# Optimization experiments

Hardware: AMD Instinct MI355X
Metric: run time of the kernel (lower is better)

The kernel has to match this reference:

```python
import jax, jax.numpy as jnp
import numpy as np
import itertools

N_GRAPHS = 64
NODES_PER_GRAPH = 16
N_NODES = N_GRAPHS * NODES_PER_GRAPH  # 1024


def conv2d(x, w, b, stride=1):
    # x: [N, Cin, H, W], w: [Cout, Cin, 3, 3], padding=1 (same as torch Conv2d(...,3,stride,1))
    y = jax.lax.conv_general_dilated(
        x, w, (stride, stride), ((1, 1), (1, 1)),
        dimension_numbers=("NCHW", "OIHW", "NCHW"))
    return y + b[None, :, None, None]


def lrelu(x):
    return jax.nn.leaky_relu(x, 0.1)


def conv_mpn(x, edges, c1w, c1b, c2w, c2b, c3w, c3b):
    # ConvMPN: gather neighbour / non-neighbour node features, scatter_add to dst,
    # concat on channel dim, then 3 convs (no activation in between, as in source).
    n = x.shape[0]
    a, s, b = edges[:, 0], edges[:, 1], edges[:, 2]
    src = jnp.concatenate([a, b])  # bidirectional, matches torch cat([e0,e2]) / cat([e2,e0])
    dst = jnp.concatenate([b, a])
    pos = jnp.concatenate([s > 0, s > 0]).astype(x.dtype)
    neg = jnp.concatenate([s < 0, s < 0]).astype(x.dtype)
    gathered = x[src]  # [2E, C, H, W]
    neigh = jax.ops.segment_sum(gathered * pos[:, None, None, None], dst, num_segments=n)
    non = jax.ops.segment_sum(gathered * neg[:, None, None, None], dst, num_segments=n)
    h = jnp.concatenate([x, neigh, non], axis=1)  # [N, 3C, H, W]
    h = conv2d(h, c1w, c1b)
    h = conv2d(h, c2w, c2b)
    h = conv2d(h, c3w, c3b)
    return h


def setup_inputs() -> dict:
    key = jax.random.key(0)
    ks = iter(jax.random.split(key, 40))

    def p(shape):
        fan_in = int(np.prod(shape[1:])) if len(shape) > 1 else shape[0]
        return jax.random.normal(next(ks), shape, dtype=jnp.float32) / np.sqrt(fan_in)

    x = jax.random.normal(next(ks), (N_NODES, 32, 32), dtype=jnp.float32)
    t = jax.random.normal(next(ks), (N_NODES, 10), dtype=jnp.float32)

    # complete graph per sample; sign +/-1 marks neighbour vs non-neighbour
    pairs = np.array(list(itertools.combinations(range(NODES_PER_GRAPH), 2)))  # (120, 2)
    offs = np.arange(N_GRAPHS)[:, None] * NODES_PER_GRAPH
    aa = (pairs[None, :, 0] + offs).ravel()
    bb = (pairs[None, :, 1] + offs).ravel()
    rng = np.random.RandomState(0)
    sign = rng.choice(np.array([-1, 1]), size=aa.shape[0])
    edges = jnp.asarray(np.stack([aa, sign, bb], axis=1).astype(np.int64))
    nd_to_sample = jnp.asarray(np.repeat(np.arange(N_GRAPHS), NODES_PER_GRAPH).astype(np.int64))

    inp = {
        "x": x, "t": t, "edges": edges, "nd_to_sample": nd_to_sample,
        "w_t": p((8192, 10)), "b_t": jnp.zeros((8192,), jnp.float32),
        "c1w": p((16, 9, 3, 3)), "c1b": jnp.zeros((16,), jnp.float32),
        "c2w": p((16, 16, 3, 3)), "c2b": jnp.zeros((16,), jnp.float32),
        "c3w": p((16, 16, 3, 3)), "c3b": jnp.zeros((16,), jnp.float32),
        "m1c1w": p((32, 48, 3, 3)), "m1c1b": jnp.zeros((32,), jnp.float32),
        "m1c2w": p((32, 32, 3, 3)), "m1c2b": jnp.zeros((32,), jnp.float32),
        "m1c3w": p((16, 32, 3, 3)), "m1c3b": jnp.zeros((16,), jnp.float32),
        "ds1w": p((16, 16, 3, 3)), "ds1b": jnp.zeros((16,), jnp.float32),
        "m2c1w": p((32, 48, 3, 3)), "m2c1b": jnp.zeros((32,), jnp.float32),
        "m2c2w": p((32, 32, 3, 3)), "m2c2b": jnp.zeros((32,), jnp.float32),
        "m2c3w": p((16, 32, 3, 3)), "m2c3b": jnp.zeros((16,), jnp.float32),
        "ds2w": p((16, 16, 3, 3)), "ds2b": jnp.zeros((16,), jnp.float32),
        "d1w": p((256, 16, 3, 3)), "d1b": jnp.zeros((256,), jnp.float32),
        "d2w": p((128, 256, 3, 3)), "d2b": jnp.zeros((128,), jnp.float32),
        "d3w": p((128, 128, 3, 3)), "d3b": jnp.zeros((128,), jnp.float32),
        "pw": p((1, 128)), "pb": jnp.zeros((1,), jnp.float32),
    }
    return inp


def reference(x, t, edges, nd_to_sample,
              w_t, b_t, c1w, c1b, c2w, c2b, c3w, c3b,
              m1c1w, m1c1b, m1c2w, m1c2b, m1c3w, m1c3b, ds1w, ds1b,
              m2c1w, m2c1b, m2c2w, m2c2b, m2c3w, m2c3b, ds2w, ds2b,
              d1w, d1b, d2w, d2b, d3w, d3b, pw, pb):
    h = x.reshape(-1, 1, 32, 32)
    tt = (t @ w_t.T + b_t).reshape(-1, 8, 32, 32)
    h = jnp.concatenate([h, tt], axis=1)  # [N, 9, 32, 32]
    h = lrelu(conv2d(h, c1w, c1b))
    h = lrelu(conv2d(h, c2w, c2b))
    h = lrelu(conv2d(h, c3w, c3b))
    h = conv_mpn(h, edges, m1c1w, m1c1b, m1c2w, m1c2b, m1c3w, m1c3b)
    h = lrelu(conv2d(h, ds1w, ds1b, stride=2))  # 32 -> 16
    h = conv_mpn(h, edges, m2c1w, m2c1b, m2c2w, m2c2b, m2c3w, m2c3b)
    h = lrelu(conv2d(h, ds2w, ds2b, stride=2))  # 16 -> 8
    h = lrelu(conv2d(h, d1w, d1b, stride=2))    # 8 -> 4
    h = lrelu(conv2d(h, d2w, d2b, stride=2))    # 4 -> 2
    h = lrelu(conv2d(h, d3w, d3b, stride=2))    # 2 -> 1
    h = h.reshape(-1, h.shape[1])               # [N, 128]
    pooled = jax.ops.segment_sum(h, nd_to_sample, num_segments=N_GRAPHS)  # add_pool
    return pooled @ pw.T + pb                    # [B, 1]
```

## Files before the change

### kernel.cpp

```cpp
#include <hip/hip_runtime.h>
#include <hip/hip_bf16.h>


#define N_NODES   1024
#define N_GRAPHS  64

typedef __hip_bfloat16 bf16;
typedef __attribute__((ext_vector_type(8)))  short  short8;
typedef __attribute__((ext_vector_type(16))) float  f32x16;

__device__ __forceinline__ float bf2f(unsigned short s) {
    union { unsigned u; float f; } x; x.u = ((unsigned)s) << 16; return x.f;
}
__device__ __forceinline__ unsigned short f2bf(float f) {
    __hip_bfloat16 h = __float2bfloat16(f);
    return *reinterpret_cast<unsigned short*>(&h);
}
__device__ __forceinline__ uint4 pack8(const float* f) {
    uint4 r;
    r.x = f2bf(f[0]) | ((unsigned)f2bf(f[1]) << 16);
    r.y = f2bf(f[2]) | ((unsigned)f2bf(f[3]) << 16);
    r.z = f2bf(f[4]) | ((unsigned)f2bf(f[5]) << 16);
    r.w = f2bf(f[6]) | ((unsigned)f2bf(f[7]) << 16);
    return r;
}

template<int N>
__device__ __forceinline__ void zacc(f32x16* a) {
    #pragma unroll
    for (int i = 0; i < N; ++i)
        #pragma unroll
        for (int e = 0; e < 16; ++e) a[i][e] = 0.f;
}

template<int TPW, int NW>
__device__ __forceinline__ void mfma_rr32(
    const short* lds, int inbase, int zch,
    const unsigned short* wfb, int kkstride_sh,
    f32x16* acc, int wid, int lane)
{
    const int pxl = lane & 31, kg = lane >> 5;
    short8 wfr[9];
    #pragma unroll
    for (int kk = 0; kk < 9; ++kk)
        wfr[kk] = *(const short8*)(wfb + (size_t)kk * kkstride_sh + lane * 8);
    const int r0 = wid * TPW;
    #pragma unroll
    for (int ir = 0; ir < TPW + 2; ++ir) {
        int iy = r0 - 1 + ir;
        if (iy < 0 || iy > 31) continue;
        #pragma unroll
        for (int dx = 0; dx < 3; ++dx) {
            int ix = pxl + dx - 1;
            bool ok = (unsigned)ix < 32u;
            int chunk = ok ? (inbase + kg * 1024 + iy * 32 + ix) : zch;
            short8 B = *(const short8*)(lds + (size_t)chunk * 8);
            #pragma unroll
            for (int dy = -1; dy <= 1; ++dy) {
                constexpr int dummy = 0; (void)dummy;
                int a = ir - 1 - dy;
                if (a < 0 || a >= TPW) continue;
                acc[a] = __builtin_amdgcn_mfma_f32_32x32x16_bf16(
                    wfr[(dy + 1) * 3 + dx], B, acc[a], 0, 0, 0);
            }
        }
    }
}

template<int WIN, int WOUT, int STRIDE, int TPW, int TILES, int NW>
__device__ __forceinline__ void mfma_phase(
    const short* lds, int inbase, int zch,
    const unsigned short* wfb, int kkstride_sh,
    f32x16* acc, int wid, int lane)
{
    constexpr int NPI = WIN * WIN;
    const int pxl = lane & 31, kg = lane >> 5;
    short8 wfr[9];
    #pragma unroll
    for (int kk = 0; kk < 9; ++kk)
        wfr[kk] = *(const short8*)(wfb + (size_t)kk * kkstride_sh + lane * 8);
    #pragma unroll
    for (int t = 0; t < TPW; ++t) {
        int tile = wid * TPW + t;
        if (NW * TPW > TILES && tile >= TILES) continue;
        int oy, ox;
        if (WOUT == 32)      { oy = tile;                  ox = pxl;      }
        else if (WOUT == 16) { oy = tile * 2 + (pxl >> 4); ox = pxl & 15; }
        else                 { oy = tile * 4 + (pxl >> 3); ox = pxl & 7;  }
        #pragma unroll
        for (int kk = 0; kk < 9; ++kk) {
            int iy = STRIDE * oy + kk / 3 - 1, ix = STRIDE * ox + kk % 3 - 1;
            bool ok = ((unsigned)iy < (unsigned)WIN) && ((unsigned)ix < (unsigned)WIN);
            int chunk = ok ? (inbase + kg * NPI + iy * WIN + ix) : zch;
            acc[t] = __builtin_amdgcn_mfma_f32_32x32x16_bf16(
                wfr[kk], *(const short8*)(lds + (size_t)chunk * 8), acc[t], 0, 0, 0);
        }
    }
}

template<int WOUT, int COUT, int RELU, int TPW, int TILES, int NW, bool TOGLOBAL>
__device__ __forceinline__ void conv_epi(
    short* lds, int outbase, unsigned short* gout,
    const float* __restrict__ bias, const f32x16* acc, int wid, int lane)
{
    constexpr int NPO = WOUT * WOUT;
    const int pxl = lane & 31, kg = lane >> 5;
    #pragma unroll
    for (int t = 0; t < TPW; ++t) {
        int tile = wid * TPW + t;
        if (NW * TPW > TILES && tile >= TILES) continue;
        int oy, ox;
        if (WOUT == 32)      { oy = tile;                  ox = pxl;      }
        else if (WOUT == 16) { oy = tile * 2 + (pxl >> 4); ox = pxl & 15; }
        else                 { oy = tile * 4 + (pxl >> 3); ox = pxl & 7;  }
        int opx = oy * WOUT + ox;
        #pragma unroll
        for (int q = 0; q < COUT / 8; ++q) {
            unsigned short u[4];
            #pragma unroll
            for (int j = 0; j < 4; ++j) {
                int co = q * 8 + kg * 4 + j;
                float v = acc[t][4 * q + j] + bias[co];
                if (RELU) v = (v >= 0.f) ? v : 0.1f * v;
                u[j] = f2bf(v);
            }
            uint2 pk;
            pk.x = u[0] | ((unsigned)u[1] << 16);
            pk.y = u[2] | ((unsigned)u[3] << 16);
            if constexpr (TOGLOBAL)
                *(uint2*)(gout + ((size_t)q * NPO + opx) * 8 + kg * 4) = pk;
            else
                *(uint2*)(lds + ((size_t)(outbase + q * NPO + opx)) * 8 + kg * 4) = pk;
        }
    }
}

__global__ __launch_bounds__(64) void k_build_adj(
    const int* __restrict__ edges, int per_g,
    int* __restrict__ cnt, int* __restrict__ lst)
{
    int n = blockIdx.x * 64 + threadIdx.x;
    if (n >= N_NODES) return;
    int g = n >> 4;
    const int* eg = edges + (size_t)g * per_g * 3;
    int c = 0;
    for (int k = 0; k < per_g; ++k) {
        int a = eg[k * 3 + 0];
        int s = eg[k * 3 + 1];
        int b = eg[k * 3 + 2];
        int other = (a == n) ? b : ((b == n) ? a : -1);
        if (other >= 0 && (other >> 4) == g && c < 16) {
            lst[n * 16 + c] = other | ((s < 0) ? (int)0x80000000 : 0);
            ++c;
        }
    }
    cnt[n] = c;
}

#define N_PREP 14
struct PrepArgs {
    const float* w[N_PREP];
    unsigned short* o[N_PREP];
    int cin[N_PREP], cout[N_PREP], cig[N_PREP], mt[N_PREP], base[N_PREP];
};

__global__ __launch_bounds__(64) void k_prep_all(PrepArgs a)
{
    int b = blockIdx.x;
    int L = 0;
    #pragma unroll
    for (int i = 1; i < N_PREP; ++i) if (b >= a.base[i]) L = i;
    int rel = b - a.base[L];
    int MT = a.mt[L], CIG = a.cig[L];
    int m = rel % MT; rel /= MT;
    int cg = rel % CIG;
    int kk = rel / CIG;
    int Cin = a.cin[L], Cout = a.cout[L];
    int lane = threadIdx.x;
    int co = m * 32 + (lane & 31), kg = lane >> 5;
    float v[8];
    #pragma unroll
    for (int j = 0; j < 8; ++j) {
        int ci = cg * 16 + kg * 8 + j;
        v[j] = (co < Cout && ci < Cin) ? a.w[L][((size_t)co * Cin + ci) * 9 + kk] : 0.f;
    }
    *(uint4*)(a.o[L] + ((size_t)((kk * CIG + cg) * MT + m) * 64 + lane) * 8) = pack8(v);
}

__global__ __launch_bounds__(512) void k_front(
    const float* __restrict__ x, const float* __restrict__ t,
    const float* __restrict__ wt, const float* __restrict__ bt,
    const unsigned short* __restrict__ wf1, const float* __restrict__ b1,
    const unsigned short* __restrict__ wf2, const float* __restrict__ b2,
    const unsigned short* __restrict__ wf3, const float* __restrict__ b3,
    bf16* __restrict__ c3o, int node_base)
{
    __shared__ __align__(16) short lds[4097 * 8];
    __shared__ float s_t[10];
    const int nl = blockIdx.x, n = node_base + nl, tid = threadIdx.x;
    const int wid = tid >> 6, lane = tid & 63;
    if (tid < 10) s_t[tid] = t[n * 10 + tid];
    if (tid < 8)  lds[4096 * 8 + tid] = 0;
    __syncthreads();

    #pragma unroll
    for (int p = 0; p < 2; ++p) {
        int px = tid + p * 512;
        float ch[16];
        ch[0] = x[(size_t)n * 1024 + px];
        #pragma unroll
        for (int c = 1; c <= 8; ++c) {
            int o = (c - 1) * 1024 + px;
            float a = bt[o];
            const float* wr = wt + (size_t)o * 10;
            #pragma unroll
            for (int k = 0; k < 10; ++k) a += wr[k] * s_t[k];
            ch[c] = a;
        }
        #pragma unroll
        for (int c = 9; c < 16; ++c) ch[c] = 0.f;
        *(uint4*)(lds + (size_t)px * 8)          = pack8(ch);
        *(uint4*)(lds + (size_t)(1024 + px) * 8) = pack8(ch + 8);
    }
    __syncthreads();

    f32x16 acc[4];
    zacc<4>(acc);
    mfma_rr32<4, 8>(lds, 0, 4096, wf1, 512, acc, wid, lane);
    conv_epi<32, 16, 1, 4, 32, 8, false>(lds, 2048, nullptr, b1, acc, wid, lane);
    __syncthreads();
    zacc<4>(acc);
    mfma_rr32<4, 8>(lds, 2048, 4096, wf2, 512, acc, wid, lane);
    conv_epi<32, 16, 1, 4, 32, 8, false>(lds, 0, nullptr, b2, acc, wid, lane);
    __syncthreads();
    zacc<4>(acc);
    mfma_rr32<4, 8>(lds, 0, 4096, wf3, 512, acc, wid, lane);
    conv_epi<32, 16, 1, 4, 32, 8, true>(lds, 0,
        (unsigned short*)c3o + (size_t)nl * 16384, b3, acc, wid, lane);
}

__global__ __launch_bounds__(512) void k_mid1(
    const bf16* __restrict__ c3o, const bf16* __restrict__ g1p,
    const unsigned short* __restrict__ wf1, const float* __restrict__ b1,
    const unsigned short* __restrict__ wf2, const float* __restrict__ b2,
    const unsigned short* __restrict__ wf3, const float* __restrict__ b3,
    const unsigned short* __restrict__ wfd, const float* __restrict__ bd,
    bf16* __restrict__ ds1o)
{
    __shared__ __align__(16) short lds[8193 * 8];
    const int nl = blockIdx.x, tid = threadIdx.x;
    const int wid = tid >> 6, lane = tid & 63;
    if (tid < 8) lds[8192 * 8 + tid] = 0;

    uint4* l4 = (uint4*)lds;
    const uint4* s0 = (const uint4*)c3o + (size_t)nl * 2048;
    const uint4* s1 = (const uint4*)g1p + (size_t)nl * 4096;
    const uint4* s2 = s1 + 2048;
    #pragma unroll
    for (int r = 0; r < 4; ++r) l4[tid + r * 512] = s0[tid + r * 512];
    __syncthreads();

    f32x16 acc[4];
    zacc<4>(acc);
    uint4 pf[4];
    #pragma unroll
    for (int r = 0; r < 4; ++r) pf[r] = s1[tid + r * 512];
    mfma_rr32<4, 8>(lds, 0, 8192, wf1, 3 * 512, acc, wid, lane);
    #pragma unroll
    for (int r = 0; r < 4; ++r) l4[2048 + tid + r * 512] = pf[r];
    __syncthreads();
    #pragma unroll
    for (int r = 0; r < 4; ++r) pf[r] = s2[tid + r * 512];
    mfma_rr32<4, 8>(lds, 2048, 8192, wf1 + 512, 3 * 512, acc, wid, lane);
    #pragma unroll
    for (int r = 0; r < 4; ++r) l4[tid + r * 512] = pf[r];
    __syncthreads();
    mfma_rr32<4, 8>(lds, 0, 8192, wf1 + 1024, 3 * 512, acc, wid, lane);
    conv_epi<32, 32, 0, 4, 32, 8, false>(lds, 4096, nullptr, b1, acc, wid, lane);
    __syncthreads();

    zacc<4>(acc);
    mfma_rr32<4, 8>(lds, 4096, 8192, wf2,       2 * 512, acc, wid, lane);
    mfma_rr32<4, 8>(lds, 6144, 8192, wf2 + 512, 2 * 512, acc, wid, lane);
    conv_epi<32, 32, 0, 4, 32, 8, false>(lds, 0, nullptr, b2, acc, wid, lane);
    __syncthreads();

    zacc<4>(acc);
    mfma_rr32<4, 8>(lds, 0,    8192, wf3,       2 * 512, acc, wid, lane);
    mfma_rr32<4, 8>(lds, 2048, 8192, wf3 + 512, 2 * 512, acc, wid, lane);
    conv_epi<32, 16, 0, 4, 32, 8, false>(lds, 4096, nullptr, b3, acc, wid, lane);
    __syncthreads();

    zacc<1>(acc);
    mfma_phase<32, 16, 2, 1, 8, 8>(lds, 4096, 8192, wfd, 512, acc, wid, lane);
    conv_epi<16, 16, 1, 1, 8, 8, true>(lds, 0,
        (unsigned short*)ds1o + (size_t)nl * 4096, bd, acc, wid, lane);
}

__global__ __launch_bounds__(512) void k_mid2(
    const bf16* __restrict__ ds1o, const bf16* __restrict__ g2p,
    const unsigned short* __restrict__ wf1, const float* __restrict__ b1,
    const unsigned short* __restrict__ wf2, const float* __restrict__ b2,
    const unsigned short* __restrict__ wf3, const float* __restrict__ b3,
    const unsigned short* __restrict__ wfd, const float* __restrict__ bd,
    bf16* __restrict__ ds2o)
{
    __shared__ __align__(16) short lds[2049 * 8];
    const int nl = blockIdx.x, tid = threadIdx.x;
    const int wid = tid >> 6, lane = tid & 63;
    if (tid < 8) lds[2048 * 8 + tid] = 0;

    uint4* l4 = (uint4*)lds;
    const uint4* s0 = (const uint4*)ds1o + (size_t)nl * 512;
    const uint4* s1 = (const uint4*)g2p + (size_t)nl * 1024;
    const uint4* s2 = s1 + 512;
    l4[tid] = s0[tid];
    __syncthreads();

    f32x16 acc[1];
    zacc<1>(acc);
    uint4 pf;
    pf = s1[tid];
    mfma_phase<16, 16, 1, 1, 8, 8>(lds, 0, 2048, wf1, 3 * 512, acc, wid, lane);
    l4[512 + tid] = pf;
    __syncthreads();
    pf = s2[tid];
    mfma_phase<16, 16, 1, 1, 8, 8>(lds, 512, 2048, wf1 + 512, 3 * 512, acc, wid, lane);
    l4[tid] = pf;
    __syncthreads();
    mfma_phase<16, 16, 1, 1, 8, 8>(lds, 0, 2048, wf1 + 1024, 3 * 512, acc, wid, lane);
    conv_epi<16, 32, 0, 1, 8, 8, false>(lds, 1024, nullptr, b1, acc, wid, lane);
    __syncthreads();

    zacc<1>(acc);
    mfma_phase<16, 16, 1, 1, 8, 8>(lds, 1024, 2048, wf2,       2 * 512, acc, wid, lane);
    mfma_phase<16, 16, 1, 1, 8, 8>(lds, 1536, 2048, wf2 + 512, 2 * 512, acc, wid, lane);
    conv_epi<16, 32, 0, 1, 8, 8, false>(lds, 0, nullptr, b2, acc, wid, lane);
    __syncthreads();

    zacc<1>(acc);
    mfma_phase<16, 16, 1, 1, 8, 8>(lds, 0,   2048, wf3,       2 * 512, acc, wid, lane);
    mfma_phase<16, 16, 1, 1, 8, 8>(lds, 512, 2048, wf3 + 512, 2 * 512, acc, wid, lane);
    conv_epi<16, 16, 0, 1, 8, 8, false>(lds, 1024, nullptr, b3, acc, wid, lane);
    __syncthreads();

    zacc<1>(acc);
    mfma_phase<16, 8, 2, 1, 2, 8>(lds, 1024, 2048, wfd, 512, acc, wid, lane);
    conv_epi<8, 16, 1, 1, 2, 8, true>(lds, 0,
        (unsigned short*)ds2o + (size_t)nl * 1024, bd, acc, wid, lane);
}

template<int NPIX>
__global__ __launch_bounds__(256) void k_gather2(
    const bf16* __restrict__ in, const int* __restrict__ cnt,
    const int* __restrict__ lst, bf16* __restrict__ out, int node_base)
{
    constexpr int CPN = 2 * NPIX;
    __shared__ __align__(16) uint4 s_in[16 * 128];
    __shared__ int s_pos[16], s_neg[16];

    const int gl = blockIdx.x, sp = blockIdx.y, tid = threadIdx.x;
    const int gn0 = node_base + gl * 16, nl0 = gl * 16;

    if (tid < 16) {
        int c = cnt[gn0 + tid]; if (c > 16) c = 16;
        int pm = 0, nm = 0;
        for (int k = 0; k < c; ++k) {
            int e = lst[(size_t)(gn0 + tid) * 16 + k];
            int sl = (e & 0x7FFFFFFF) - gn0;
            if ((unsigned)sl < 16u) { if (e < 0) nm |= 1 << sl; else pm |= 1 << sl; }
        }
        s_pos[tid] = pm; s_neg[tid] = nm;
    }
    const uint4* in4 = (const uint4*)in;
    for (int i = tid; i < 2048; i += 256) {
        int srcn = i >> 7, chk = i & 127;
        s_in[i] = in4[(size_t)(nl0 + srcn) * CPN + sp * 128 + chk];
    }
    __syncthreads();

    const int dh = tid >> 7, ch = tid & 127;
    int pm[8], nm[8];
    #pragma unroll
    for (int dl = 0; dl < 8; ++dl) {
        pm[dl] = __builtin_amdgcn_readfirstlane(s_pos[dh * 8 + dl]);
        nm[dl] = __builtin_amdgcn_readfirstlane(s_neg[dh * 8 + dl]);
    }

    float aP[8][8], aN[8][8];
    #pragma unroll
    for (int dl = 0; dl < 8; ++dl)
        #pragma unroll
        for (int j = 0; j < 8; ++j) { aP[dl][j] = 0.f; aN[dl][j] = 0.f; }

    for (int s = 0; s < 16; ++s) {
        union { uint4 v; unsigned short u[8]; } q;
        q.v = s_in[s * 128 + ch];
        float f[8];
        #pragma unroll
        for (int j = 0; j < 8; ++j) f[j] = bf2f(q.u[j]);
        #pragma unroll
        for (int dl = 0; dl < 8; ++dl) {
            if ((pm[dl] >> s) & 1) {
                #pragma unroll
                for (int j = 0; j < 8; ++j) aP[dl][j] += f[j];
            }
            if ((nm[dl] >> s) & 1) {
                #pragma unroll
                for (int j = 0; j < 8; ++j) aN[dl][j] += f[j];
            }
        }
    }

    uint4* out4 = (uint4*)out;
    #pragma unroll
    for (int dl = 0; dl < 8; ++dl) {
        int d = nl0 + dh * 8 + dl;
        out4[((size_t)d * 2 + 0) * CPN + sp * 128 + ch] = pack8(aP[dl]);
        out4[((size_t)d * 2 + 1) * CPN + sp * 128 + ch] = pack8(aN[dl]);
    }
}

template<int HIN, int CIG, int COUT, int IPB, int FUSE_POOL>
__global__ __launch_bounds__(256) void k_tail(
    const bf16* __restrict__ in, const unsigned short* __restrict__ wf,
    const float* __restrict__ bias, bf16* __restrict__ out,
    const int* __restrict__ nd, const float* __restrict__ pw,
    float* __restrict__ pool_out, int nc, int node_base)
{
    constexpr int HOUT = HIN / 2, NPO = HOUT * HOUT, NPI = HIN * HIN;
    constexpr int MT  = (COUT + 31) / 32;
    constexpr int NT  = (IPB * NPO) / 32;
    constexpr int TOT = MT * NT;
    constexpr int TPW = TOT / 4;
    static_assert(TOT % 4 == 0, "tile count must divide over 4 waves");
    constexpr int CHUNKS = IPB * 2 * CIG * NPI;
    __shared__ __align__(16) short sbuf[CHUNKS * 8 + 8];

    const int tid = threadIdx.x, wid = tid >> 6, lane = tid & 63;
    const int col = lane & 31, kg = lane >> 5;
    const int img0 = blockIdx.x * IPB;

    {
        const uint4* src = (const uint4*)in + (size_t)img0 * (2 * CIG * NPI);
        uint4* dst = (uint4*)sbuf;
        int nav = nc - img0; if (nav > IPB) nav = IPB;
        int nch = nav * 2 * CIG * NPI;
        uint4 z = {0, 0, 0, 0};
        for (int i = tid; i < CHUNKS; i += 256) dst[i] = (i < nch) ? src[i] : z;
        if (tid < 8) sbuf[CHUNKS * 8 + tid] = 0;
    }
    __syncthreads();

    int imgb[TPW], poff[TPW][9];
    #pragma unroll
    for (int t = 0; t < TPW; ++t) {
        int tl = wid + 4 * t;
        int n  = tl % NT;
        int idx = n * 32 + col;
        int img = idx / NPO, px = idx % NPO;
        imgb[t] = img * (2 * CIG * NPI);
        int oy = px / HOUT, ox = px % HOUT;
        #pragma unroll
        for (int kk = 0; kk < 9; ++kk) {
            int iy = 2 * oy + kk / 3 - 1, ix = 2 * ox + kk % 3 - 1;
            bool ok = ((unsigned)iy < (unsigned)HIN) && ((unsigned)ix < (unsigned)HIN);
            poff[t][kk] = ok ? (iy * HIN + ix) : -1;
        }
    }

    f32x16 acc[TPW];
    #pragma unroll
    for (int t = 0; t < TPW; ++t)
        #pragma unroll
        for (int e = 0; e < 16; ++e) acc[t][e] = 0.f;

    for (int cig = 0; cig < CIG; ++cig) {
        #pragma unroll
        for (int t = 0; t < TPW; ++t) {
            int m = (wid + 4 * t) / NT;
            #pragma unroll
            for (int kk = 0; kk < 9; ++kk) {
                short8 wfr = *(const short8*)(wf +
                    ((size_t)((kk * CIG + cig) * MT + m) * 64 + lane) * 8);
                int chunk = (poff[t][kk] >= 0)
                          ? imgb[t] + (cig * 2 + kg) * NPI + poff[t][kk]
                          : CHUNKS;
                acc[t] = __builtin_amdgcn_mfma_f32_32x32x16_bf16(
                            wfr, *(const short8*)(sbuf + chunk * 8), acc[t], 0, 0, 0);
            }
        }
    }

    #pragma unroll
    for (int t = 0; t < TPW; ++t) {
        int tl = wid + 4 * t;
        int m = tl / NT, n = tl % NT;
        int idx = n * 32 + col;
        int img = idx / NPO, px = idx % NPO;
        bool live = (img0 + img) < nc;
        if (FUSE_POOL) {
            float part = 0.f;
            #pragma unroll
            for (int r = 0; r < 16; ++r) {
                int co = m * 32 + (r & 3) + 8 * (r >> 2) + 4 * kg;
                float v = acc[t][r] + bias[co];
                v = (v >= 0.f) ? v : 0.1f * v;
                part += v * pw[co];
            }
            part += __shfl_xor(part, 32, 64);
            if (kg == 0 && live) {
                int g = nd[node_base + img0 + img];
                if (g < 0) g = 0; if (g >= N_GRAPHS) g = N_GRAPHS - 1;
                atomicAdd(&pool_out[g], part);
            }
        } else if (live) {
            unsigned short* outp = (unsigned short*)out;
            #pragma unroll
            for (int q = 0; q < 4; ++q) {
                if (m * 32 + q * 8 < COUT) {
                    unsigned short u[4];
                    #pragma unroll
                    for (int j = 0; j < 4; ++j) {
                        int co = m * 32 + q * 8 + kg * 4 + j;
                        float v = acc[t][4 * q + j] + bias[co];
                        v = (v >= 0.f) ? v : 0.1f * v;
                        u[j] = f2bf(v);
                    }
                    uint2 pk;
                    pk.x = u[0] | ((unsigned)u[1] << 16);
                    pk.y = u[2] | ((unsigned)u[3] << 16);
                    *(uint2*)(outp + (((size_t)(img0 + img) * (COUT / 8)
                              + (m * 4 + q)) * NPO + px) * 8 + kg * 4) = pk;
                }
            }
        }
    }
}

__global__ void k_init_out(float* out, const float* __restrict__ pb)
{
    int i = threadIdx.x;
    if (i < N_GRAPHS) out[i] = pb[0];
}

extern "C" void kernel_launch(void* const* d_in, const int* in_sizes, int n_in,
                              void* d_out, int out_size, void* d_ws, size_t ws_size,
                              hipStream_t stream)
{
    const float* x     = (const float*)d_in[0];
    const float* t     = (const float*)d_in[1];
    const int*   edges = (const int*)d_in[2];
    const int*   nd    = (const int*)d_in[3];
    const float* w_t   = (const float*)d_in[4];
    const float* b_t   = (const float*)d_in[5];
    const float* c1w   = (const float*)d_in[6];
    const float* c1b   = (const float*)d_in[7];
    const float* c2w   = (const float*)d_in[8];
    const float* c2b   = (const float*)d_in[9];
    const float* c3w   = (const float*)d_in[10];
    const float* c3b   = (const float*)d_in[11];
    const float* m1c1w = (const float*)d_in[12];
    const float* m1c1b = (const float*)d_in[13];
    const float* m1c2w = (const float*)d_in[14];
    const float* m1c2b = (const float*)d_in[15];
    const float* m1c3w = (const float*)d_in[16];
    const float* m1c3b = (const float*)d_in[17];
    const float* ds1w  = (const float*)d_in[18];
    const float* ds1b  = (const float*)d_in[19];
    const float* m2c1w = (const float*)d_in[20];
    const float* m2c1b = (const float*)d_in[21];
    const float* m2c2w = (const float*)d_in[22];
    const float* m2c2b = (const float*)d_in[23];
    const float* m2c3w = (const float*)d_in[24];
    const float* m2c3b = (const float*)d_in[25];
    const float* ds2w  = (const float*)d_in[26];
    const float* ds2b  = (const float*)d_in[27];
    const float* d1w   = (const float*)d_in[28];
    const float* d1b   = (const float*)d_in[29];
    const float* d2w   = (const float*)d_in[30];
    const float* d2b   = (const float*)d_in[31];
    const float* d3w   = (const float*)d_in[32];
    const float* d3b   = (const float*)d_in[33];
    const float* pw    = (const float*)d_in[34];
    const float* pb    = (const float*)d_in[35];
    float* out = (float*)d_out;

    uint8_t* ws = (uint8_t*)d_ws;
    int* adj_cnt = (int*)ws;
    int* adj_lst = (int*)(ws + 4096);
    #define WF(i)  ((unsigned short*)(ws + (128u << 10) + (size_t)(i) * 32768))
    unsigned short* wt_ds1 = (unsigned short*)(ws + (416u  << 10));
    unsigned short* wt_ds2 = (unsigned short*)(ws + (428u  << 10));
    unsigned short* wt_d1  = (unsigned short*)(ws + (440u  << 10));
    unsigned short* wt_d2  = (unsigned short*)(ws + (512u  << 10));
    unsigned short* wt_d3  = (unsigned short*)(ws + (1088u << 10));

    const size_t RESV = 2ull << 20;
    size_t avail = (ws_size > RESV) ? ws_size - RESV : 0;
    int ncap = (int)(avail / (120 * 1024));
    ncap = (ncap / 16) * 16;
    if (ncap < 16) ncap = 16;
    if (ncap > N_NODES) ncap = N_NODES;
    uint8_t* R = ws + RESV;
    #define NB(off_kb) (R + (size_t)(off_kb) * 1024 * ncap)

    bf16*  c3o  = (bf16*)NB(0);
    bf16*  g1p  = (bf16*)NB(32);
    bf16*  ds1o = (bf16*)NB(96);
    bf16*  g2p  = (bf16*)NB(104);
    bf16*  ds2o = (bf16*)NB(0);
    bf16*  d1o  = (bf16*)NB(2);
    bf16*  d2o  = (bf16*)NB(10);

    int nE    = in_sizes[2] / 3;
    int per_g = nE / N_GRAPHS;

    k_build_adj<<<(N_NODES + 63) / 64, 64, 0, stream>>>(edges, per_g, adj_cnt, adj_lst);
    k_init_out<<<1, 64, 0, stream>>>(out, pb);

    {
        PrepArgs pa;
        const float* wsrc[N_PREP] = { c1w, c2w, c3w, m1c1w, m1c2w, m1c3w,
                                      m2c1w, m2c2w, m2c3w, ds1w, ds2w,
                                      d1w, d2w, d3w };
        unsigned short* wdst[N_PREP] = { WF(0), WF(1), WF(2), WF(3), WF(4), WF(5),
                                         WF(6), WF(7), WF(8), wt_ds1, wt_ds2,
                                         wt_d1, wt_d2, wt_d3 };
        int cin_[N_PREP]  = { 9, 16, 16, 48, 32, 32, 48, 32, 32, 16, 16, 16, 256, 128 };
        int cout_[N_PREP] = { 16, 16, 16, 32, 32, 16, 32, 32, 16, 16, 16, 256, 128, 128 };
        int cig_[N_PREP]  = { 1, 1, 1, 3, 2, 2, 3, 2, 2, 1, 1, 1, 16, 8 };
        int mt_[N_PREP]   = { 1, 1, 1, 1, 1, 1, 1, 1, 1, 1, 1, 8, 4, 4 };
        int total = 0;
        for (int i = 0; i < N_PREP; ++i) {
            pa.w[i] = wsrc[i]; pa.o[i] = wdst[i];
            pa.cin[i] = cin_[i]; pa.cout[i] = cout_[i];
            pa.cig[i] = cig_[i]; pa.mt[i] = mt_[i];
            pa.base[i] = total;
            total += 9 * cig_[i] * mt_[i];
        }
        k_prep_all<<<total, 64, 0, stream>>>(pa);
    }

    for (int nb = 0; nb < N_NODES; nb += ncap) {
        int nc = (N_NODES - nb < ncap) ? (N_NODES - nb) : ncap;
        int ng = nc / 16;

        k_front<<<nc, 512, 0, stream>>>(x, t, w_t, b_t,
            WF(0), c1b, WF(1), c2b, WF(2), c3b, c3o, nb);

        k_gather2<1024><<<dim3(ng, 16), 256, 0, stream>>>(c3o, adj_cnt, adj_lst, g1p, nb);

        k_mid1<<<nc, 512, 0, stream>>>(c3o, g1p,
            WF(3), m1c1b, WF(4), m1c2b, WF(5), m1c3b, wt_ds1, ds1b, ds1o);

        k_gather2<256><<<dim3(ng, 4), 256, 0, stream>>>(ds1o, adj_cnt, adj_lst, g2p, nb);

        k_mid2<<<nc, 512, 0, stream>>>(ds1o, g2p,
            WF(6), m2c1b, WF(7), m2c2b, WF(8), m2c3b, wt_ds2, ds2b, ds2o);

        k_tail<8, 1, 256, 4, 0><<<(nc + 3) / 4, 256, 0, stream>>>(
            ds2o, wt_d1, d1b, d1o, nullptr, nullptr, nullptr, nc, nb);
        k_tail<4, 16, 128, 8, 0><<<(nc + 7) / 8, 256, 0, stream>>>(
            d1o, wt_d2, d2b, d2o, nullptr, nullptr, nullptr, nc, nb);
        k_tail<2, 8, 128, 32, 1><<<(nc + 31) / 32, 256, 0, stream>>>(
            d2o, wt_d3, d3b, nullptr, nd, pw, out, nc, nb);
    }
    #undef NB
    #undef WF
}
```

Measured before the change: 285.3 us.

## Fuse tail convs into one kernel, merge setup kernels, use async LDS loads

```diff
diff --git a/kernel.cpp b/kernel.cpp
--- a/kernel.cpp
+++ b/kernel.cpp
@@ -12,17 +12,26 @@
 __device__ __forceinline__ float bf2f(unsigned short s) {
     union { unsigned u; float f; } x; x.u = ((unsigned)s) << 16; return x.f;
 }
-__device__ __forceinline__ unsigned short f2bf(float f) {
-    __hip_bfloat16 h = __float2bfloat16(f);
-    return *reinterpret_cast<unsigned short*>(&h);
+__device__ __forceinline__ unsigned cvtpk(float a, float b) {
+    unsigned r;
+    asm("v_cvt_pk_bf16_f32 %0, %1, %2" : "=v"(r) : "v"(a), "v"(b));
+    return r;
 }
 __device__ __forceinline__ uint4 pack8(const float* f) {
     uint4 r;
-    r.x = f2bf(f[0]) | ((unsigned)f2bf(f[1]) << 16);
-    r.y = f2bf(f[2]) | ((unsigned)f2bf(f[3]) << 16);
-    r.z = f2bf(f[4]) | ((unsigned)f2bf(f[5]) << 16);
-    r.w = f2bf(f[6]) | ((unsigned)f2bf(f[7]) << 16);
+    r.x = cvtpk(f[0], f[1]);
+    r.y = cvtpk(f[2], f[3]);
+    r.z = cvtpk(f[4], f[5]);
+    r.w = cvtpk(f[6], f[7]);
     return r;
+}
+__device__ __forceinline__ void gload16(const void* g, void* l) {
+    __builtin_amdgcn_global_load_lds(
+        reinterpret_cast<const __attribute__((address_space(1))) unsigned*>(
+            reinterpret_cast<uintptr_t>(g)),
+        reinterpret_cast<__attribute__((address_space(3))) unsigned*>(
+            reinterpret_cast<uintptr_t>(l)),
+        16, 0, 0);
 }
 
 template<int N>
@@ -31,40 +40,6 @@
     for (int i = 0; i < N; ++i)
         #pragma unroll
         for (int e = 0; e < 16; ++e) a[i][e] = 0.f;
-}
-
-template<int TPW, int NW>
-__device__ __forceinline__ void mfma_rr32(
-    const short* lds, int inbase, int zch,
-    const unsigned short* wfb, int kkstride_sh,
-    f32x16* acc, int wid, int lane)
-{
-    const int pxl = lane & 31, kg = lane >> 5;
-    short8 wfr[9];
-    #pragma unroll
-    for (int kk = 0; kk < 9; ++kk)
-        wfr[kk] = *(const short8*)(wfb + (size_t)kk * kkstride_sh + lane * 8);
-    const int r0 = wid * TPW;
-    #pragma unroll
-    for (int ir = 0; ir < TPW + 2; ++ir) {
-        int iy = r0 - 1 + ir;
-        if (iy < 0 || iy > 31) continue;
-        #pragma unroll
-        for (int dx = 0; dx < 3; ++dx) {
-            int ix = pxl + dx - 1;
-            bool ok = (unsigned)ix < 32u;
-            int chunk = ok ? (inbase + kg * 1024 + iy * 32 + ix) : zch;
-            short8 B = *(const short8*)(lds + (size_t)chunk * 8);
-            #pragma unroll
-            for (int dy = -1; dy <= 1; ++dy) {
-                constexpr int dummy = 0; (void)dummy;
-                int a = ir - 1 - dy;
-                if (a < 0 || a >= TPW) continue;
-                acc[a] = __builtin_amdgcn_mfma_f32_32x32x16_bf16(
-                    wfr[(dy + 1) * 3 + dx], B, acc[a], 0, 0, 0);
-            }
-        }
-    }
 }
 
 template<int WIN, int WOUT, int STRIDE, int TPW, int TILES, int NW>
@@ -116,45 +91,22 @@
         int opx = oy * WOUT + ox;
         #pragma unroll
         for (int q = 0; q < COUT / 8; ++q) {
-            unsigned short u[4];
+            float v[4];
             #pragma unroll
             for (int j = 0; j < 4; ++j) {
                 int co = q * 8 + kg * 4 + j;
-                float v = acc[t][4 * q + j] + bias[co];
-                if (RELU) v = (v >= 0.f) ? v : 0.1f * v;
-                u[j] = f2bf(v);
+                float x = acc[t][4 * q + j] + bias[co];
+                v[j] = RELU ? ((x >= 0.f) ? x : 0.1f * x) : x;
             }
             uint2 pk;
-            pk.x = u[0] | ((unsigned)u[1] << 16);
-            pk.y = u[2] | ((unsigned)u[3] << 16);
+            pk.x = cvtpk(v[0], v[1]);
+            pk.y = cvtpk(v[2], v[3]);
             if constexpr (TOGLOBAL)
                 *(uint2*)(gout + ((size_t)q * NPO + opx) * 8 + kg * 4) = pk;
             else
                 *(uint2*)(lds + ((size_t)(outbase + q * NPO + opx)) * 8 + kg * 4) = pk;
         }
     }
-}
-
-__global__ __launch_bounds__(64) void k_build_adj(
-    const int* __restrict__ edges, int per_g,
-    int* __restrict__ cnt, int* __restrict__ lst)
-{
-    int n = blockIdx.x * 64 + threadIdx.x;
-    if (n >= N_NODES) return;
-    int g = n >> 4;
-    const int* eg = edges + (size_t)g * per_g * 3;
-    int c = 0;
-    for (int k = 0; k < per_g; ++k) {
-        int a = eg[k * 3 + 0];
-        int s = eg[k * 3 + 1];
-        int b = eg[k * 3 + 2];
-        int other = (a == n) ? b : ((b == n) ? a : -1);
-        if (other >= 0 && (other >> 4) == g && c < 16) {
-            lst[n * 16 + c] = other | ((s < 0) ? (int)0x80000000 : 0);
-            ++c;
-        }
-    }
-    cnt[n] = c;
 }
 
 #define N_PREP 14
@@ -162,29 +114,53 @@
     const float* w[N_PREP];
     unsigned short* o[N_PREP];
     int cin[N_PREP], cout[N_PREP], cig[N_PREP], mt[N_PREP], base[N_PREP];
+    int prep_total;
+    const int* edges; int per_g;
+    int* adj_cnt; int* adj_lst;
+    float* out; const float* pb;
 };
 
-__global__ __launch_bounds__(64) void k_prep_all(PrepArgs a)
+__global__ __launch_bounds__(64) void k_setup(PrepArgs a)
 {
     int b = blockIdx.x;
-    int L = 0;
-    #pragma unroll
-    for (int i = 1; i < N_PREP; ++i) if (b >= a.base[i]) L = i;
-    int rel = b - a.base[L];
-    int MT = a.mt[L], CIG = a.cig[L];
-    int m = rel % MT; rel /= MT;
-    int cg = rel % CIG;
-    int kk = rel / CIG;
-    int Cin = a.cin[L], Cout = a.cout[L];
-    int lane = threadIdx.x;
-    int co = m * 32 + (lane & 31), kg = lane >> 5;
-    float v[8];
-    #pragma unroll
-    for (int j = 0; j < 8; ++j) {
-        int ci = cg * 16 + kg * 8 + j;
-        v[j] = (co < Cout && ci < Cin) ? a.w[L][((size_t)co * Cin + ci) * 9 + kk] : 0.f;
-    }
-    *(uint4*)(a.o[L] + ((size_t)((kk * CIG + cg) * MT + m) * 64 + lane) * 8) = pack8(v);
+    int tid = threadIdx.x;
+    if (b < a.prep_total) {
+        int L = 0;
+        #pragma unroll
+        for (int i = 1; i < N_PREP; ++i) if (b >= a.base[i]) L = i;
+        int rel = b - a.base[L];
+        int MT = a.mt[L], CIG = a.cig[L];
+        int m = rel % MT; rel /= MT;
+        int cg = rel % CIG;
+        int kk = rel / CIG;
+        int Cin = a.cin[L], Cout = a.cout[L];
+        int co = m * 32 + (tid & 31), kg = tid >> 5;
+        float v[8];
+        #pragma unroll
+        for (int j = 0; j < 8; ++j) {
+            int ci = cg * 16 + kg * 8 + j;
+            v[j] = (co < Cout && ci < Cin) ? a.w[L][((size_t)co * Cin + ci) * 9 + kk] : 0.f;
+        }
+        *(uint4*)(a.o[L] + ((size_t)((kk * CIG + cg) * MT + m) * 64 + tid) * 8) = pack8(v);
+    } else if (b < a.prep_total + 16) {
+        int n = (b - a.prep_total) * 64 + tid;
+        int g = n >> 4;
+        const int* eg = a.edges + (size_t)g * a.per_g * 3;
+        int c = 0;
+        for (int k = 0; k < a.per_g; ++k) {
+            int aa = eg[k * 3 + 0];
+            int s  = eg[k * 3 + 1];
+            int bb = eg[k * 3 + 2];
+            int other = (aa == n) ? bb : ((bb == n) ? aa : -1);
+            if (other >= 0 && (other >> 4) == g && c < 16) {
+                a.adj_lst[n * 16 + c] = other | ((s < 0) ? (int)0x80000000 : 0);
+                ++c;
+            }
+        }
+        a.adj_cnt[n] = c;
+    } else {
+        if (tid < N_GRAPHS) a.out[tid] = a.pb[0];
+    }
 }
 
 __global__ __launch_bounds__(512) void k_front(
@@ -226,15 +202,15 @@
 
     f32x16 acc[4];
     zacc<4>(acc);
-    mfma_rr32<4, 8>(lds, 0, 4096, wf1, 512, acc, wid, lane);
+    mfma_phase<32, 32, 1, 4, 32, 8>(lds, 0, 4096, wf1, 512, acc, wid, lane);
     conv_epi<32, 16, 1, 4, 32, 8, false>(lds, 2048, nullptr, b1, acc, wid, lane);
     __syncthreads();
     zacc<4>(acc);
-    mfma_rr32<4, 8>(lds, 2048, 4096, wf2, 512, acc, wid, lane);
+    mfma_phase<32, 32, 1, 4, 32, 8>(lds, 2048, 4096, wf2, 512, acc, wid, lane);
     conv_epi<32, 16, 1, 4, 32, 8, false>(lds, 0, nullptr, b2, acc, wid, lane);
     __syncthreads();
     zacc<4>(acc);
-    mfma_rr32<4, 8>(lds, 0, 4096, wf3, 512, acc, wid, lane);
+    mfma_phase<32, 32, 1, 4, 32, 8>(lds, 0, 4096, wf3, 512, acc, wid, lane);
     conv_epi<32, 16, 1, 4, 32, 8, true>(lds, 0,
         (unsigned short*)c3o + (size_t)nl * 16384, b3, acc, wid, lane);
 }
@@ -265,29 +241,29 @@
     uint4 pf[4];
     #pragma unroll
     for (int r = 0; r < 4; ++r) pf[r] = s1[tid + r * 512];
-    mfma_rr32<4, 8>(lds, 0, 8192, wf1, 3 * 512, acc, wid, lane);
+    mfma_phase<32, 32, 1, 4, 32, 8>(lds, 0, 8192, wf1, 3 * 512, acc, wid, lane);
     #pragma unroll
     for (int r = 0; r < 4; ++r) l4[2048 + tid + r * 512] = pf[r];
     __syncthreads();
     #pragma unroll
     for (int r = 0; r < 4; ++r) pf[r] = s2[tid + r * 512];
-    mfma_rr32<4, 8>(lds, 2048, 8192, wf1 + 512, 3 * 512, acc, wid, lane);
+    mfma_phase<32, 32, 1, 4, 32, 8>(lds, 2048, 8192, wf1 + 512, 3 * 512, acc, wid, lane);
     #pragma unroll
     for (int r = 0; r < 4; ++r) l4[tid + r * 512] = pf[r];
     __syncthreads();
-    mfma_rr32<4, 8>(lds, 0, 8192, wf1 + 1024, 3 * 512, acc, wid, lane);
+    mfma_phase<32, 32, 1, 4, 32, 8>(lds, 0, 8192, wf1 + 1024, 3 * 512, acc, wid, lane);
     conv_epi<32, 32, 0, 4, 32, 8, false>(lds, 4096, nullptr, b1, acc, wid, lane);
     __syncthreads();
 
     zacc<4>(acc);
-    mfma_rr32<4, 8>(lds, 4096, 8192, wf2,       2 * 512, acc, wid, lane);
-    mfma_rr32<4, 8>(lds, 6144, 8192, wf2 + 512, 2 * 512, acc, wid, lane);
+    mfma_phase<32, 32, 1, 4, 32, 8>(lds, 4096, 8192, wf2,       2 * 512, acc, wid, lane);
+    mfma_phase<32, 32, 1, 4, 32, 8>(lds, 6144, 8192, wf2 + 512, 2 * 512, acc, wid, lane);
     conv_epi<32, 32, 0, 4, 32, 8, false>(lds, 0, nullptr, b2, acc, wid, lane);
     __syncthreads();
 
     zacc<4>(acc);
-    mfma_rr32<4, 8>(lds, 0,    8192, wf3,       2 * 512, acc, wid, lane);
-    mfma_rr32<4, 8>(lds, 2048, 8192, wf3 + 512, 2 * 512, acc, wid, lane);
+    mfma_phase<32, 32, 1, 4, 32, 8>(lds, 0,    8192, wf3,       2 * 512, acc, wid, lane);
+    mfma_phase<32, 32, 1, 4, 32, 8>(lds, 2048, 8192, wf3 + 512, 2 * 512, acc, wid, lane);
     conv_epi<32, 16, 0, 4, 32, 8, false>(lds, 4096, nullptr, b3, acc, wid, lane);
     __syncthreads();
 
@@ -373,9 +349,11 @@
         s_pos[tid] = pm; s_neg[tid] = nm;
     }
     const uint4* in4 = (const uint4*)in;
-    for (int i = tid; i < 2048; i += 256) {
+    #pragma unroll
+    for (int k = 0; k < 8; ++k) {
+        int i = tid + k * 256;
         int srcn = i >> 7, chk = i & 127;
-        s_in[i] = in4[(size_t)(nl0 + srcn) * CPN + sp * 128 + chk];
+        gload16(&in4[(size_t)(nl0 + srcn) * CPN + sp * 128 + chk], &s_in[i]);
     }
     __syncthreads();
 
@@ -421,127 +399,157 @@
     }
 }
 
-template<int HIN, int CIG, int COUT, int IPB, int FUSE_POOL>
-__global__ __launch_bounds__(256) void k_tail(
-    const bf16* __restrict__ in, const unsigned short* __restrict__ wf,
-    const float* __restrict__ bias, bf16* __restrict__ out,
+__global__ __launch_bounds__(512) void k_tail3(
+    const bf16* __restrict__ ds2o,
+    const unsigned short* __restrict__ w1, const float* __restrict__ b1,
+    const unsigned short* __restrict__ w2, const float* __restrict__ b2,
+    const unsigned short* __restrict__ w3, const float* __restrict__ b3,
     const int* __restrict__ nd, const float* __restrict__ pw,
-    float* __restrict__ pool_out, int nc, int node_base)
-{
-    constexpr int HOUT = HIN / 2, NPO = HOUT * HOUT, NPI = HIN * HIN;
-    constexpr int MT  = (COUT + 31) / 32;
-    constexpr int NT  = (IPB * NPO) / 32;
-    constexpr int TOT = MT * NT;
-    constexpr int TPW = TOT / 4;
-    static_assert(TOT % 4 == 0, "tile count must divide over 4 waves");
-    constexpr int CHUNKS = IPB * 2 * CIG * NPI;
-    __shared__ __align__(16) short sbuf[CHUNKS * 8 + 8];
-
+    float* __restrict__ out, int node_base)
+{
+    __shared__ __align__(16) short lds[5121 * 8];
+    __shared__ float s_part[4][8];
     const int tid = threadIdx.x, wid = tid >> 6, lane = tid & 63;
     const int col = lane & 31, kg = lane >> 5;
-    const int img0 = blockIdx.x * IPB;
+    const int img0 = blockIdx.x * 8;
+    if (tid < 8) lds[5120 * 8 + tid] = 0;
+
+    const uint4* src = (const uint4*)ds2o + (size_t)img0 * 128;
+    gload16(src + tid,       (uint4*)lds + tid);
+    gload16(src + 512 + tid, (uint4*)lds + 512 + tid);
+    __syncthreads();
 
     {
-        const uint4* src = (const uint4*)in + (size_t)img0 * (2 * CIG * NPI);
-        uint4* dst = (uint4*)sbuf;
-        int nav = nc - img0; if (nav > IPB) nav = IPB;
-        int nch = nav * 2 * CIG * NPI;
-        uint4 z = {0, 0, 0, 0};
-        for (int i = tid; i < CHUNKS; i += 256) dst[i] = (i < nch) ? src[i] : z;
-        if (tid < 8) sbuf[CHUNKS * 8 + tid] = 0;
-    }
-    __syncthreads();
-
-    int imgb[TPW], poff[TPW][9];
-    #pragma unroll
-    for (int t = 0; t < TPW; ++t) {
-        int tl = wid + 4 * t;
-        int n  = tl % NT;
-        int idx = n * 32 + col;
-        int img = idx / NPO, px = idx % NPO;
-        imgb[t] = img * (2 * CIG * NPI);
-        int oy = px / HOUT, ox = px % HOUT;
+        f32x16 acc[4];
+        zacc<4>(acc);
+        #pragma unroll
+        for (int t = 0; t < 4; ++t) {
+            int tl = wid + 8 * t;
+            int m = tl >> 2, n = tl & 3;
+            int idx = n * 32 + col;
+            int img = idx >> 4, px = idx & 15;
+            int oy = px >> 2, ox = px & 3;
+            #pragma unroll
+            for (int kk = 0; kk < 9; ++kk) {
+                int iy = 2 * oy + kk / 3 - 1, ix = 2 * ox + kk % 3 - 1;
+                bool ok = ((unsigned)iy < 8u) && ((unsigned)ix < 8u);
+                int chunk = ok ? (img * 128 + kg * 64 + iy * 8 + ix) : 5120;
+                short8 wfr = *(const short8*)(w1 + ((size_t)(kk * 8 + m) * 64 + lane) * 8);
+                acc[t] = __builtin_amdgcn_mfma_f32_32x32x16_bf16(
+                    wfr, *(const short8*)(lds + (size_t)chunk * 8), acc[t], 0, 0, 0);
+            }
+        }
+        #pragma unroll
+        for (int t = 0; t < 4; ++t) {
+            int tl = wid + 8 * t;
+            int m = tl >> 2, n = tl & 3;
+            int idx = n * 32 + col;
+            int img = idx >> 4, px = idx & 15;
+            #pragma unroll
+            for (int q = 0; q < 4; ++q) {
+                float v[4];
+                #pragma unroll
+                for (int j = 0; j < 4; ++j) {
+                    int co = m * 32 + q * 8 + kg * 4 + j;
+                    float x = acc[t][4 * q + j] + b1[co];
+                    v[j] = (x >= 0.f) ? x : 0.1f * x;
+                }
+                uint2 pk;
+                pk.x = cvtpk(v[0], v[1]);
+                pk.y = cvtpk(v[2], v[3]);
+                *(uint2*)(lds + ((size_t)(1024 + img * 512 + (m * 4 + q) * 16 + px)) * 8
+                          + kg * 4) = pk;
+            }
+        }
+    }
+    __syncthreads();
+
+    {
+        f32x16 acc;
+        #pragma unroll
+        for (int e = 0; e < 16; ++e) acc[e] = 0.f;
+        int img = col >> 2, px = col & 3;
+        int oy = px >> 1, ox = px & 1;
+        int poff[9];
         #pragma unroll
         for (int kk = 0; kk < 9; ++kk) {
             int iy = 2 * oy + kk / 3 - 1, ix = 2 * ox + kk % 3 - 1;
-            bool ok = ((unsigned)iy < (unsigned)HIN) && ((unsigned)ix < (unsigned)HIN);
-            poff[t][kk] = ok ? (iy * HIN + ix) : -1;
-        }
-    }
-
-    f32x16 acc[TPW];
-    #pragma unroll
-    for (int t = 0; t < TPW; ++t)
-        #pragma unroll
-        for (int e = 0; e < 16; ++e) acc[t][e] = 0.f;
-
-    for (int cig = 0; cig < CIG; ++cig) {
-        #pragma unroll
-        for (int t = 0; t < TPW; ++t) {
-            int m = (wid + 4 * t) / NT;
+            bool ok = ((unsigned)iy < 4u) && ((unsigned)ix < 4u);
+            poff[kk] = ok ? (iy * 4 + ix) : -1;
+        }
+        if (wid < 4) {
+            for (int cig = 0; cig < 16; ++cig) {
+                #pragma unroll
+                for (int kk = 0; kk < 9; ++kk) {
+                    short8 wfr = *(const short8*)(w2 +
+                        ((size_t)((kk * 16 + cig) * 4 + wid) * 64 + lane) * 8);
+                    int chunk = (poff[kk] >= 0)
+                              ? 1024 + img * 512 + (cig * 2 + kg) * 16 + poff[kk]
+                              : 5120;
+                    acc = __builtin_amdgcn_mfma_f32_32x32x16_bf16(
+                        wfr, *(const short8*)(lds + (size_t)chunk * 8), acc, 0, 0, 0);
+                }
+            }
+        }
+        __syncthreads();
+        if (wid < 4) {
             #pragma unroll
-            for (int kk = 0; kk < 9; ++kk) {
-                short8 wfr = *(const short8*)(wf +
-                    ((size_t)((kk * CIG + cig) * MT + m) * 64 + lane) * 8);
-                int chunk = (poff[t][kk] >= 0)
-                          ? imgb[t] + (cig * 2 + kg) * NPI + poff[t][kk]
-                          : CHUNKS;
-                acc[t] = __builtin_amdgcn_mfma_f32_32x32x16_bf16(
-                            wfr, *(const short8*)(sbuf + chunk * 8), acc[t], 0, 0, 0);
-            }
-        }
-    }
-
-    #pragma unroll
-    for (int t = 0; t < TPW; ++t) {
-        int tl = wid + 4 * t;
-        int m = tl / NT, n = tl % NT;
-        int idx = n * 32 + col;
-        int img = idx / NPO, px = idx % NPO;
-        bool live = (img0 + img) < nc;
-        if (FUSE_POOL) {
+            for (int q = 0; q < 4; ++q) {
+                float v[4];
+                #pragma unroll
+                for (int j = 0; j < 4; ++j) {
+                    int co = wid * 32 + q * 8 + kg * 4 + j;
+                    float x = acc[4 * q + j] + b2[co];
+                    v[j] = (x >= 0.f) ? x : 0.1f * x;
+                }
+                uint2 pk;
+                pk.x = cvtpk(v[0], v[1]);
+                pk.y = cvtpk(v[2], v[3]);
+                *(uint2*)(lds + ((size_t)(img * 64 + (wid * 4 + q) * 4 + px)) * 8
+                          + kg * 4) = pk;
+            }
+        }
+    }
+    __syncthreads();
+
+    {
+        if (wid < 4) {
+            int img = col;
+            bool live = col < 8;
+            f32x16 acc;
+            #pragma unroll
+            for (int e = 0; e < 16; ++e) acc[e] = 0.f;
+            for (int cig = 0; cig < 8; ++cig) {
+                #pragma unroll
+                for (int kk = 0; kk < 9; ++kk) {
+                    int iy = kk / 3 - 1, ix = kk % 3 - 1;
+                    bool ok = live && ((unsigned)iy < 2u) && ((unsigned)ix < 2u);
+                    int chunk = ok ? (img * 64 + (cig * 2 + kg) * 4 + iy * 2 + ix) : 5120;
+                    short8 wfr = *(const short8*)(w3 +
+                        ((size_t)((kk * 8 + cig) * 4 + wid) * 64 + lane) * 8);
+                    acc = __builtin_amdgcn_mfma_f32_32x32x16_bf16(
+                        wfr, *(const short8*)(lds + (size_t)chunk * 8), acc, 0, 0, 0);
+                }
+            }
             float part = 0.f;
             #pragma unroll
             for (int r = 0; r < 16; ++r) {
-                int co = m * 32 + (r & 3) + 8 * (r >> 2) + 4 * kg;
-                float v = acc[t][r] + bias[co];
+                int co = wid * 32 + (r & 3) + 8 * (r >> 2) + 4 * kg;
+                float v = acc[r] + b3[co];
                 v = (v >= 0.f) ? v : 0.1f * v;
                 part += v * pw[co];
             }
             part += __shfl_xor(part, 32, 64);
-            if (kg == 0 && live) {
-                int g = nd[node_base + img0 + img];
-                if (g < 0) g = 0; if (g >= N_GRAPHS) g = N_GRAPHS - 1;
-                atomicAdd(&pool_out[g], part);
-            }
-        } else if (live) {
-            unsigned short* outp = (unsigned short*)out;
-            #pragma unroll
-            for (int q = 0; q < 4; ++q) {
-                if (m * 32 + q * 8 < COUT) {
-                    unsigned short u[4];
-                    #pragma unroll
-                    for (int j = 0; j < 4; ++j) {
-                        int co = m * 32 + q * 8 + kg * 4 + j;
-                        float v = acc[t][4 * q + j] + bias[co];
-                        v = (v >= 0.f) ? v : 0.1f * v;
-                        u[j] = f2bf(v);
-                    }
-                    uint2 pk;
-                    pk.x = u[0] | ((unsigned)u[1] << 16);
-                    pk.y = u[2] | ((unsigned)u[3] << 16);
-                    *(uint2*)(outp + (((size_t)(img0 + img) * (COUT / 8)
-                              + (m * 4 + q)) * NPO + px) * 8 + kg * 4) = pk;
-                }
-            }
-        }
-    }
-}
-
-__global__ void k_init_out(float* out, const float* __restrict__ pb)
-{
-    int i = threadIdx.x;
-    if (i < N_GRAPHS) out[i] = pb[0];
+            if (kg == 0 && live) s_part[wid][col] = part;
+        }
+        __syncthreads();
+        if (tid < 8) {
+            float s = s_part[0][tid] + s_part[1][tid] + s_part[2][tid] + s_part[3][tid];
+            int g = nd[node_base + img0 + tid];
+            if (g < 0) g = 0; if (g >= N_GRAPHS) g = N_GRAPHS - 1;
+            atomicAdd(&out[g], s);
+        }
+    }
 }
 
 extern "C" void kernel_launch(void* const* d_in, const int* in_sizes, int n_in,
@@ -610,14 +618,9 @@
     bf16*  ds1o = (bf16*)NB(96);
     bf16*  g2p  = (bf16*)NB(104);
     bf16*  ds2o = (bf16*)NB(0);
-    bf16*  d1o  = (bf16*)NB(2);
-    bf16*  d2o  = (bf16*)NB(10);
 
     int nE    = in_sizes[2] / 3;
     int per_g = nE / N_GRAPHS;
-
-    k_build_adj<<<(N_NODES + 63) / 64, 64, 0, stream>>>(edges, per_g, adj_cnt, adj_lst);
-    k_init_out<<<1, 64, 0, stream>>>(out, pb);
 
     {
         PrepArgs pa;
@@ -639,7 +642,11 @@
             pa.base[i] = total;
             total += 9 * cig_[i] * mt_[i];
         }
-        k_prep_all<<<total, 64, 0, stream>>>(pa);
+        pa.prep_total = total;
+        pa.edges = edges; pa.per_g = per_g;
+        pa.adj_cnt = adj_cnt; pa.adj_lst = adj_lst;
+        pa.out = out; pa.pb = pb;
+        k_setup<<<total + 16 + 1, 64, 0, stream>>>(pa);
     }
 
     for (int nb = 0; nb < N_NODES; nb += ncap) {
@@ -659,12 +666,8 @@
         k_mid2<<<nc, 512, 0, stream>>>(ds1o, g2p,
             WF(6), m2c1b, WF(7), m2c2b, WF(8), m2c3b, wt_ds2, ds2b, ds2o);
 
-        k_tail<8, 1, 256, 4, 0><<<(nc + 3) / 4, 256, 0, stream>>>(
-            ds2o, wt_d1, d1b, d1o, nullptr, nullptr, nullptr, nc, nb);
-        k_tail<4, 16, 128, 8, 0><<<(nc + 7) / 8, 256, 0, stream>>>(
-            d1o, wt_d2, d2b, d2o, nullptr, nullptr, nullptr, nc, nb);
-        k_tail<2, 8, 128, 32, 1><<<(nc + 31) / 32, 256, 0, stream>>>(
-            d2o, wt_d3, d3b, nullptr, nd, pw, out, nc, nb);
+        k_tail3<<<nc / 8, 512, 0, stream>>>(ds2o,
+            wt_d1, d1b, wt_d2, d2b, wt_d3, d3b, nd, pw, out, nb);
     }
     #undef NB
     #undef WF
```

Measured after the change: 246.4 us (median of 2 runs). 13.6% less time.
